# Optimization experiments

Hardware: AMD Instinct MI355X
Metric: run time of the kernel (lower is better)

The kernel has to match this reference:

```python
import jax, jax.numpy as jnp
import numpy as np

B, H, S, D = 2, 16, 2048, 128
SPARSITY = 0.1
NEG = -1.0e9


def local_mask(seq_len: int) -> jnp.ndarray:
    # window_size = max(1, int(seq_len * sparsity)); row i keeps cols [i-w//2, i+w//2]
    w = max(1, int(seq_len * SPARSITY))
    half = w // 2
    idx = jnp.arange(seq_len)
    diff = idx[None, :] - idx[:, None]  # j - i
    return ((diff >= -half) & (diff <= half)).astype(jnp.float32)


def setup_inputs() -> dict:
    key = jax.random.key(0)
    kq, kk, kv = jax.random.split(key, 3)
    return {
        "query": jax.random.normal(kq, (B, H, S, D), dtype=jnp.float32),
        "key": jax.random.normal(kk, (B, H, S, D), dtype=jnp.float32),
        "value": jax.random.normal(kv, (B, H, S, D), dtype=jnp.float32),
    }


def reference(query, key, value):
    head_dim = query.shape[-1]
    seq_len_k = key.shape[2]
    m = local_mask(seq_len_k)[None, None]  # [1,1,S,S]
    scores = jnp.einsum("bhqd,bhkd->bhqk", query, key) / jnp.sqrt(
        jnp.asarray(head_dim, query.dtype)
    )
    scores = scores * m + (1.0 - m) * NEG
    probs = jax.nn.softmax(scores, axis=-1)
    context = jnp.einsum("bhqk,bhkd->bhqd", probs, value)
    return context, probs
```

## Files before the change

kernel.cpp:

```cpp
#include <hip/hip_runtime.h>
#include <math.h>


namespace {
constexpr int Sc = 2048, Dc = 128;
constexpr int HALFW = 102;
constexpr float SCALE = 0.08838834764831845f;
constexpr int TQ  = 32;
constexpr int CT  = 256;
constexpr int KST = 136;
constexpr int VST = 132;
constexpr int PTS = 36;
constexpr int OFF_KBUF = 0;
constexpr int OFF_PST  = 34816;
constexpr int OFF_QS   = 34816;
constexpr int OFF_RED  = 34816 + 36864;
constexpr int LDS_TOTAL = OFF_RED + 512 + 128 + 128;
}

typedef __bf16 bf16x8 __attribute__((ext_vector_type(8)));
typedef float  f32x16 __attribute__((ext_vector_type(16)));
typedef float  fx4    __attribute__((ext_vector_type(4)));

__device__ __forceinline__ unsigned short f2bf(float f) {
    unsigned u = __float_as_uint(f);
    u += 0x7fffu + ((u >> 16) & 1u);
    return (unsigned short)(u >> 16);
}

__global__ __launch_bounds__(256, 2) void sparse_attn_mfma(
    const float* __restrict__ Q, const float* __restrict__ K,
    const float* __restrict__ V, float* __restrict__ ctx,
    float* __restrict__ probs)
{
    __shared__ __align__(16) unsigned char smem[LDS_TOTAL];
    unsigned short* Ks   = (unsigned short*)(smem + OFF_KBUF);
    float*          Vsf  = (float*)(smem + OFF_KBUF);
    float*          Ps_t = (float*)(smem + OFF_PST);
    unsigned short* Qs   = (unsigned short*)(smem + OFF_QS);
    float (*red)[4]      = (float(*)[4])(smem + OFF_RED);
    float* rowM          = (float*)(smem + OFF_RED + 512);
    float* rowSinv       = (float*)(smem + OFF_RED + 512 + 128);

    const int tid  = threadIdx.x;
    const int lane = tid & 63;
    const int w    = tid >> 6;
    const int lo   = lane & 31;
    const int hi   = lane >> 5;

    const int wid = (blockIdx.x & 7) * 256 + (blockIdx.x >> 3);
    const int bh  = wid >> 6;
    const int qt  = wid & 63;
    const int i0  = qt * TQ;
    const int js0 = max(0, i0 - HALFW);
    const int jend = min(js0 + CT, Sc);

    const size_t rowbase = (size_t)bh * Sc;
    float* probsBase = probs + (rowbase + i0) * (size_t)Sc;

    {
        const int headN = js0 & 3;
        const int tailN = (4 - (jend & 3)) & 3;
        const int hn = headN + tailN;
        if (hn == 4) {
            int r = tid >> 2, s = tid & 3;
            if (r < TQ) {
                int col = (s < headN) ? (js0 - headN + s) : (jend + s - headN);
                __builtin_nontemporal_store(0.0f, probsBase + (size_t)r * Sc + col);
            }
        } else if (hn == 2) {
            int r = tid >> 1, s = tid & 1;
            if (r < TQ) {
                int col = (s < headN) ? (js0 - headN + s) : (jend + s - headN);
                __builtin_nontemporal_store(0.0f, probsBase + (size_t)r * Sc + col);
            }
        }
        const int leftQ   = (js0 - headN) >> 2;
        const int rightQ0 = (jend + tailN) >> 2;
        const fx4 z4 = {0.f, 0.f, 0.f, 0.f};
        for (int r = 0; r < TQ; ++r) {
            fx4* p4 = (fx4*)(probsBase + (size_t)r * Sc);
            for (int c = tid; c < leftQ; c += 256)
                __builtin_nontemporal_store(z4, p4 + c);
            for (int c = rightQ0 + tid; c < Sc / 4; c += 256)
                __builtin_nontemporal_store(z4, p4 + c);
        }
    }

    {
        const float4* Q4 = (const float4*)(Q + (rowbase + i0) * Dc);
        #pragma unroll
        for (int it = 0; it < 4; ++it) {
            int idx = tid + 256 * it;
            int r = idx >> 5, d4 = idx & 31;
            float4 q4 = Q4[r * 32 + d4];
            ushort4 b;
            b.x = f2bf(q4.x); b.y = f2bf(q4.y); b.z = f2bf(q4.z); b.w = f2bf(q4.w);
            *(ushort4*)&Qs[r * KST + d4 * 4] = b;
        }
    }

    const float4* K4 = (const float4*)(K + rowbase * Dc);
    const float4* V4 = (const float4*)(V + rowbase * Dc);

    f32x16 accE[2];
    #pragma unroll
    for (int ch = 0; ch < 2; ++ch) {
        #pragma unroll
        for (int it = 0; it < 16; ++it) {
            int idx = tid + 256 * it;
            int r = idx >> 5, d4 = idx & 31;
            int jn = js0 + ch * 128 + r;
            if (jn > Sc - 1) jn = Sc - 1;
            float4 k4 = K4[(size_t)jn * 32 + d4];
            ushort4 b;
            b.x = f2bf(k4.x); b.y = f2bf(k4.y); b.z = f2bf(k4.z); b.w = f2bf(k4.w);
            *(ushort4*)&Ks[r * KST + d4 * 4] = b;
        }
        __syncthreads();
        f32x16 acc;
        #pragma unroll
        for (int i = 0; i < 16; ++i) acc[i] = 0.0f;
        const unsigned short* qrow = &Qs[lo * KST + hi * 8];
        const unsigned short* krow = &Ks[(w * 32 + lo) * KST + hi * 8];
        #pragma unroll
        for (int dk = 0; dk < 8; ++dk) {
            bf16x8 a = *(const bf16x8*)(qrow + dk * 16);
            bf16x8 b = *(const bf16x8*)(krow + dk * 16);
            acc = __builtin_amdgcn_mfma_f32_32x32x16_bf16(a, b, acc, 0, 0, 0);
        }
        accE[ch] = acc;
        __syncthreads();
    }

    const int cg0 = js0 + w * 32 + lo;
    {
        float mred[16];
        #pragma unroll
        for (int i = 0; i < 16; ++i) {
            int rl = (i & 3) + 8 * (i >> 2) + 4 * hi;
            int rg = i0 + rl;
            float m = -3.0e38f;
            #pragma unroll
            for (int ch = 0; ch < 2; ++ch) {
                int cg = cg0 + ch * 128;
                bool valid = (cg < Sc) & (cg >= rg - HALFW) & (cg <= rg + HALFW);
                float sv = valid ? accE[ch][i] * SCALE : -3.0e38f;
                accE[ch][i] = sv;
                m = fmaxf(m, sv);
            }
            mred[i] = m;
        }
        #pragma unroll
        for (int mk = 1; mk < 32; mk <<= 1) {
            #pragma unroll
            for (int i = 0; i < 16; ++i)
                mred[i] = fmaxf(mred[i], __shfl_xor(mred[i], mk, 64));
        }
        if (lo == 0) {
            #pragma unroll
            for (int i = 0; i < 16; ++i) {
                int rl = (i & 3) + 8 * (i >> 2) + 4 * hi;
                red[rl][w] = mred[i];
            }
        }
    }
    __syncthreads();
    if (tid < 128) {
        int rr = tid >> 2, sl = tid & 3;
        float v = red[rr][sl];
        v = fmaxf(v, __shfl_xor(v, 1, 64));
        v = fmaxf(v, __shfl_xor(v, 2, 64));
        if (sl == 0) rowM[rr] = v;
    }
    __syncthreads();

    {
        float sred[16];
        #pragma unroll
        for (int i = 0; i < 16; ++i) {
            int rl = (i & 3) + 8 * (i >> 2) + 4 * hi;
            float rm = rowM[rl];
            float e0 = __expf(accE[0][i] - rm);
            float e1 = __expf(accE[1][i] - rm);
            accE[0][i] = e0; accE[1][i] = e1;
            sred[i] = e0 + e1;
        }
        #pragma unroll
        for (int mk = 1; mk < 32; mk <<= 1) {
            #pragma unroll
            for (int i = 0; i < 16; ++i)
                sred[i] += __shfl_xor(sred[i], mk, 64);
        }
        if (lo == 0) {
            #pragma unroll
            for (int i = 0; i < 16; ++i) {
                int rl = (i & 3) + 8 * (i >> 2) + 4 * hi;
                red[rl][w] = sred[i];
            }
        }
    }
    __syncthreads();
    if (tid < 128) {
        int rr = tid >> 2, sl = tid & 3;
        float v = red[rr][sl];
        v += __shfl_xor(v, 1, 64);
        v += __shfl_xor(v, 2, 64);
        if (sl == 0) rowSinv[rr] = 1.0f / v;
    }
    __syncthreads();

    #pragma unroll
    for (int i = 0; i < 16; ++i) {
        int rl = (i & 3) + 8 * (i >> 2) + 4 * hi;
        float inv = rowSinv[rl];
        float* prow = probsBase + (size_t)rl * Sc;
        #pragma unroll
        for (int ch = 0; ch < 2; ++ch) {
            int cg = cg0 + ch * 128;
            float p = accE[ch][i] * inv;
            Ps_t[(cg - js0) * PTS + rl] = p;
            if (cg < Sc) __builtin_nontemporal_store(p, prow + cg);
        }
    }
    __syncthreads();

    const int kp  = lane & 3;
    const int dgq = (lane >> 2) & 1;
    const int rg  = lane >> 3;
    fx4 o[4][4];
    #pragma unroll
    for (int c = 0; c < 4; ++c)
        #pragma unroll
        for (int j = 0; j < 4; ++j) o[c][j] = (fx4){0.f, 0.f, 0.f, 0.f};

    #pragma unroll
    for (int ch4 = 0; ch4 < 4; ++ch4) {
        #pragma unroll
        for (int it = 0; it < 8; ++it) {
            int idx = tid + 256 * it;
            int r = idx >> 5, d4 = idx & 31;
            int jn = js0 + ch4 * 64 + r;
            if (jn > Sc - 1) jn = Sc - 1;
            float4 v4g = V4[(size_t)jn * 32 + d4];
            *(float4*)&Vsf[r * VST + d4 * 4] = v4g;
        }
        __syncthreads();
        const float* Pbase = &Ps_t[(ch4 * 64) * PTS + 4 * rg];
        const float* Vbase = &Vsf[w * 32 + dgq * 16];
        #pragma unroll 4
        for (int kk = 0; kk < 16; ++kk) {
            int k = 4 * kk + kp;
            fx4 p4 = *(const fx4*)(Pbase + k * PTS);
            const float* vr = Vbase + k * VST;
            fx4 v0 = *(const fx4*)(vr);
            fx4 v1 = *(const fx4*)(vr + 4);
            fx4 v2 = *(const fx4*)(vr + 8);
            fx4 v3 = *(const fx4*)(vr + 12);
            #pragma unroll
            for (int c = 0; c < 4; ++c) {
                float pc = p4[c];
                o[c][0] += v0 * pc;
                o[c][1] += v1 * pc;
                o[c][2] += v2 * pc;
                o[c][3] += v3 * pc;
            }
        }
        __syncthreads();
    }

    #pragma unroll
    for (int c = 0; c < 4; ++c) {
        #pragma unroll
        for (int j = 0; j < 4; ++j) {
            fx4 t = o[c][j];
            #pragma unroll
            for (int comp = 0; comp < 4; ++comp) {
                float s = t[comp];
                s += __shfl_xor(s, 1, 64);
                s += __shfl_xor(s, 2, 64);
                t[comp] = s;
            }
            o[c][j] = t;
        }
    }
    if (kp == 0) {
        #pragma unroll
        for (int c = 0; c < 4; ++c) {
            float* crow = ctx + (rowbase + i0 + 4 * rg + c) * (size_t)Dc
                        + w * 32 + dgq * 16;
            #pragma unroll
            for (int j = 0; j < 4; ++j)
                __builtin_nontemporal_store(o[c][j], (fx4*)crow + j);
        }
    }
}

extern "C" void kernel_launch(void* const* d_in, const int* in_sizes, int n_in,
                              void* d_out, int out_size, void* d_ws, size_t ws_size,
                              hipStream_t stream) {
    const float* Q = (const float*)d_in[0];
    const float* K = (const float*)d_in[1];
    const float* V = (const float*)d_in[2];
    float* out   = (float*)d_out;
    float* ctx   = out;
    float* probs = out + (size_t)2 * 16 * 2048 * 128;

    dim3 grid(2 * 16 * (Sc / TQ));
    dim3 block(256);
    sparse_attn_mfma<<<grid, block, 0, stream>>>(Q, K, V, ctx, probs);
}
```

Measured before the change: 692.9 us.

## Shrink LDS footprint and raise occupancy; keep Q in registers, store P as bf16

Q is now converted straight into MFMA A-operand registers, so its LDS staging buffer goes away. P is stored transposed in LDS as bf16, and V is streamed in 32-row chunks into a separate region, which shrinks LDS to about 35KB and allows launch bounds of 4 blocks per CU. The large zero-fill of the probs array moves to the end of the kernel so it can overlap with other blocks' compute, and barriers become a waitcnt+s_barrier asm. The trade-offs are lower precision for P in the PV product, tighter register pressure from the extra occupancy target, and more barriers from the doubled V chunk count.

```diff
diff --git a/kernel.cpp b/kernel.cpp
--- a/kernel.cpp
+++ b/kernel.cpp
@@ -11,33 +11,40 @@
 constexpr int KST = 136;
 constexpr int VST = 132;
 constexpr int PTS = 36;
-constexpr int OFF_KBUF = 0;
-constexpr int OFF_PST  = 34816;
-constexpr int OFF_QS   = 34816;
-constexpr int OFF_RED  = 34816 + 36864;
-constexpr int LDS_TOTAL = OFF_RED + 512 + 128 + 128;
+constexpr int OFF_PST = 0;
+constexpr int OFF_VSF = 18432;
+constexpr int SLAB    = 35328;
+constexpr int OFF_RED = SLAB;
+constexpr int LDS_TOTAL = SLAB + 512 + 128 + 128;
 }
 
 typedef __bf16 bf16x8 __attribute__((ext_vector_type(8)));
 typedef float  f32x16 __attribute__((ext_vector_type(16)));
 typedef float  fx4    __attribute__((ext_vector_type(4)));
+typedef unsigned short u16x8 __attribute__((ext_vector_type(8)));
+typedef unsigned short u16x4 __attribute__((ext_vector_type(4)));
 
 __device__ __forceinline__ unsigned short f2bf(float f) {
     unsigned u = __float_as_uint(f);
     u += 0x7fffu + ((u >> 16) & 1u);
     return (unsigned short)(u >> 16);
 }
-
-__global__ __launch_bounds__(256, 2) void sparse_attn_mfma(
+__device__ __forceinline__ float bf2f(unsigned short h) {
+    return __uint_as_float(((unsigned)h) << 16);
+}
+__device__ __forceinline__ void bar_lds() {
+    asm volatile("s_waitcnt lgkmcnt(0)\n\ts_barrier" ::: "memory");
+}
+
+__global__ __launch_bounds__(256, 4) void sparse_attn_mfma(
     const float* __restrict__ Q, const float* __restrict__ K,
     const float* __restrict__ V, float* __restrict__ ctx,
     float* __restrict__ probs)
 {
     __shared__ __align__(16) unsigned char smem[LDS_TOTAL];
-    unsigned short* Ks   = (unsigned short*)(smem + OFF_KBUF);
-    float*          Vsf  = (float*)(smem + OFF_KBUF);
-    float*          Ps_t = (float*)(smem + OFF_PST);
-    unsigned short* Qs   = (unsigned short*)(smem + OFF_QS);
+    unsigned short* Ks   = (unsigned short*)(smem);
+    unsigned short* Ps_t = (unsigned short*)(smem + OFF_PST);
+    float*          Vsf  = (float*)(smem + OFF_VSF);
     float (*red)[4]      = (float(*)[4])(smem + OFF_RED);
     float* rowM          = (float*)(smem + OFF_RED + 512);
     float* rowSinv       = (float*)(smem + OFF_RED + 512 + 128);
@@ -57,6 +64,213 @@
 
     const size_t rowbase = (size_t)bh * Sc;
     float* probsBase = probs + (rowbase + i0) * (size_t)Sc;
+
+    const float4* K4 = (const float4*)(K + rowbase * Dc);
+    const float4* V4 = (const float4*)(V + rowbase * Dc);
+
+    bf16x8 aq[8];
+    {
+        const float4* Q4 = (const float4*)(Q + (rowbase + i0) * Dc);
+        #pragma unroll 2
+        for (int dk = 0; dk < 8; ++dk) {
+            float4 a = Q4[lo * 32 + dk * 4 + hi * 2];
+            float4 b = Q4[lo * 32 + dk * 4 + hi * 2 + 1];
+            u16x8 t;
+            t[0] = f2bf(a.x); t[1] = f2bf(a.y); t[2] = f2bf(a.z); t[3] = f2bf(a.w);
+            t[4] = f2bf(b.x); t[5] = f2bf(b.y); t[6] = f2bf(b.z); t[7] = f2bf(b.w);
+            aq[dk] = __builtin_bit_cast(bf16x8, t);
+        }
+    }
+
+    f32x16 accE[2];
+    #pragma unroll
+    for (int ch = 0; ch < 2; ++ch) {
+        #pragma unroll 4
+        for (int it = 0; it < 16; ++it) {
+            int idx = tid + 256 * it;
+            int r = idx >> 5, d4 = idx & 31;
+            int jn = js0 + ch * 128 + r;
+            if (jn > Sc - 1) jn = Sc - 1;
+            float4 k4 = K4[(size_t)jn * 32 + d4];
+            ushort4 b;
+            b.x = f2bf(k4.x); b.y = f2bf(k4.y); b.z = f2bf(k4.z); b.w = f2bf(k4.w);
+            *(ushort4*)&Ks[r * KST + d4 * 4] = b;
+        }
+        bar_lds();
+        f32x16 acc;
+        #pragma unroll
+        for (int i = 0; i < 16; ++i) acc[i] = 0.0f;
+        const unsigned short* krow = &Ks[(w * 32 + lo) * KST + hi * 8];
+        #pragma unroll
+        for (int dk = 0; dk < 8; ++dk) {
+            bf16x8 b = *(const bf16x8*)(krow + dk * 16);
+            acc = __builtin_amdgcn_mfma_f32_32x32x16_bf16(aq[dk], b, acc, 0, 0, 0);
+        }
+        accE[ch] = acc;
+        bar_lds();
+    }
+
+    const int cg0 = js0 + w * 32 + lo;
+    {
+        float mred[16];
+        #pragma unroll
+        for (int i = 0; i < 16; ++i) {
+            int rl = (i & 3) + 8 * (i >> 2) + 4 * hi;
+            int rg = i0 + rl;
+            float m = -3.0e38f;
+            #pragma unroll
+            for (int ch = 0; ch < 2; ++ch) {
+                int cg = cg0 + ch * 128;
+                bool valid = (cg < Sc) & (cg >= rg - HALFW) & (cg <= rg + HALFW);
+                float sv = valid ? accE[ch][i] * SCALE : -3.0e38f;
+                accE[ch][i] = sv;
+                m = fmaxf(m, sv);
+            }
+            mred[i] = m;
+        }
+        #pragma unroll
+        for (int mk = 1; mk < 32; mk <<= 1) {
+            #pragma unroll
+            for (int i = 0; i < 16; ++i)
+                mred[i] = fmaxf(mred[i], __shfl_xor(mred[i], mk, 64));
+        }
+        if (lo == 0) {
+            #pragma unroll
+            for (int i = 0; i < 16; ++i) {
+                int rl = (i & 3) + 8 * (i >> 2) + 4 * hi;
+                red[rl][w] = mred[i];
+            }
+        }
+    }
+    bar_lds();
+    if (tid < 128) {
+        int rr = tid >> 2, sl = tid & 3;
+        float v = red[rr][sl];
+        v = fmaxf(v, __shfl_xor(v, 1, 64));
+        v = fmaxf(v, __shfl_xor(v, 2, 64));
+        if (sl == 0) rowM[rr] = v;
+    }
+    bar_lds();
+
+    {
+        float sred[16];
+        #pragma unroll
+        for (int i = 0; i < 16; ++i) {
+            int rl = (i & 3) + 8 * (i >> 2) + 4 * hi;
+            float rm = rowM[rl];
+            float e0 = __expf(accE[0][i] - rm);
+            float e1 = __expf(accE[1][i] - rm);
+            accE[0][i] = e0; accE[1][i] = e1;
+            sred[i] = e0 + e1;
+        }
+        #pragma unroll
+        for (int mk = 1; mk < 32; mk <<= 1) {
+            #pragma unroll
+            for (int i = 0; i < 16; ++i)
+                sred[i] += __shfl_xor(sred[i], mk, 64);
+        }
+        if (lo == 0) {
+            #pragma unroll
+            for (int i = 0; i < 16; ++i) {
+                int rl = (i & 3) + 8 * (i >> 2) + 4 * hi;
+                red[rl][w] = sred[i];
+            }
+        }
+    }
+    bar_lds();
+    if (tid < 128) {
+        int rr = tid >> 2, sl = tid & 3;
+        float v = red[rr][sl];
+        v += __shfl_xor(v, 1, 64);
+        v += __shfl_xor(v, 2, 64);
+        if (sl == 0) rowSinv[rr] = 1.0f / v;
+    }
+    bar_lds();
+
+    #pragma unroll
+    for (int i = 0; i < 16; ++i) {
+        int rl = (i & 3) + 8 * (i >> 2) + 4 * hi;
+        float inv = rowSinv[rl];
+        float* prow = probsBase + (size_t)rl * Sc;
+        #pragma unroll
+        for (int ch = 0; ch < 2; ++ch) {
+            int cg = cg0 + ch * 128;
+            float p = accE[ch][i] * inv;
+            Ps_t[(cg - js0) * PTS + rl] = f2bf(p);
+            if (cg < Sc) __builtin_nontemporal_store(p, prow + cg);
+        }
+    }
+    bar_lds();
+
+    const int kp  = lane & 3;
+    const int dgq = (lane >> 2) & 1;
+    const int rg  = lane >> 3;
+    fx4 o[4][4];
+    #pragma unroll
+    for (int c = 0; c < 4; ++c)
+        #pragma unroll
+        for (int j = 0; j < 4; ++j) o[c][j] = (fx4){0.f, 0.f, 0.f, 0.f};
+
+    #pragma unroll 2
+    for (int ch8 = 0; ch8 < 8; ++ch8) {
+        #pragma unroll
+        for (int it = 0; it < 4; ++it) {
+            int idx = tid + 256 * it;
+            int r = idx >> 5, d4 = idx & 31;
+            int jn = js0 + ch8 * 32 + r;
+            if (jn > Sc - 1) jn = Sc - 1;
+            float4 v4g = V4[(size_t)jn * 32 + d4];
+            *(float4*)&Vsf[r * VST + d4 * 4] = v4g;
+        }
+        bar_lds();
+        const unsigned short* Pbase = &Ps_t[(ch8 * 32) * PTS + 4 * rg];
+        const float* Vbase = &Vsf[w * 32 + dgq * 16];
+        #pragma unroll 4
+        for (int kk = 0; kk < 8; ++kk) {
+            int k = 4 * kk + kp;
+            u16x4 pb = *(const u16x4*)(Pbase + k * PTS);
+            const float* vr = Vbase + k * VST;
+            fx4 v0 = *(const fx4*)(vr);
+            fx4 v1 = *(const fx4*)(vr + 4);
+            fx4 v2 = *(const fx4*)(vr + 8);
+            fx4 v3 = *(const fx4*)(vr + 12);
+            #pragma unroll
+            for (int c = 0; c < 4; ++c) {
+                float pc = bf2f(pb[c]);
+                o[c][0] += v0 * pc;
+                o[c][1] += v1 * pc;
+                o[c][2] += v2 * pc;
+                o[c][3] += v3 * pc;
+            }
+        }
+        bar_lds();
+    }
+
+    #pragma unroll
+    for (int c = 0; c < 4; ++c) {
+        #pragma unroll
+        for (int j = 0; j < 4; ++j) {
+            fx4 t = o[c][j];
+            #pragma unroll
+            for (int comp = 0; comp < 4; ++comp) {
+                float s = t[comp];
+                s += __shfl_xor(s, 1, 64);
+                s += __shfl_xor(s, 2, 64);
+                t[comp] = s;
+            }
+            o[c][j] = t;
+        }
+    }
+    if (kp == 0) {
+        #pragma unroll
+        for (int c = 0; c < 4; ++c) {
+            float* crow = ctx + (rowbase + i0 + 4 * rg + c) * (size_t)Dc
+                        + w * 32 + dgq * 16;
+            #pragma unroll
+            for (int j = 0; j < 4; ++j)
+                __builtin_nontemporal_store(o[c][j], (fx4*)crow + j);
+        }
+    }
 
     {
         const int headN = js0 & 3;
@@ -86,214 +300,6 @@
                 __builtin_nontemporal_store(z4, p4 + c);
         }
     }
-
-    {
-        const float4* Q4 = (const float4*)(Q + (rowbase + i0) * Dc);
-        #pragma unroll
-        for (int it = 0; it < 4; ++it) {
-            int idx = tid + 256 * it;
-            int r = idx >> 5, d4 = idx & 31;
-            float4 q4 = Q4[r * 32 + d4];
-            ushort4 b;
-            b.x = f2bf(q4.x); b.y = f2bf(q4.y); b.z = f2bf(q4.z); b.w = f2bf(q4.w);
-            *(ushort4*)&Qs[r * KST + d4 * 4] = b;
-        }
-    }
-
-    const float4* K4 = (const float4*)(K + rowbase * Dc);
-    const float4* V4 = (const float4*)(V + rowbase * Dc);
-
-    f32x16 accE[2];
-    #pragma unroll
-    for (int ch = 0; ch < 2; ++ch) {
-        #pragma unroll
-        for (int it = 0; it < 16; ++it) {
-            int idx = tid + 256 * it;
-            int r = idx >> 5, d4 = idx & 31;
-            int jn = js0 + ch * 128 + r;
-            if (jn > Sc - 1) jn = Sc - 1;
-            float4 k4 = K4[(size_t)jn * 32 + d4];
-            ushort4 b;
-            b.x = f2bf(k4.x); b.y = f2bf(k4.y); b.z = f2bf(k4.z); b.w = f2bf(k4.w);
-            *(ushort4*)&Ks[r * KST + d4 * 4] = b;
-        }
-        __syncthreads();
-        f32x16 acc;
-        #pragma unroll
-        for (int i = 0; i < 16; ++i) acc[i] = 0.0f;
-        const unsigned short* qrow = &Qs[lo * KST + hi * 8];
-        const unsigned short* krow = &Ks[(w * 32 + lo) * KST + hi * 8];
-        #pragma unroll
-        for (int dk = 0; dk < 8; ++dk) {
-            bf16x8 a = *(const bf16x8*)(qrow + dk * 16);
-            bf16x8 b = *(const bf16x8*)(krow + dk * 16);
-            acc = __builtin_amdgcn_mfma_f32_32x32x16_bf16(a, b, acc, 0, 0, 0);
-        }
-        accE[ch] = acc;
-        __syncthreads();
-    }
-
-    const int cg0 = js0 + w * 32 + lo;
-    {
-        float mred[16];
-        #pragma unroll
-        for (int i = 0; i < 16; ++i) {
-            int rl = (i & 3) + 8 * (i >> 2) + 4 * hi;
-            int rg = i0 + rl;
-            float m = -3.0e38f;
-            #pragma unroll
-            for (int ch = 0; ch < 2; ++ch) {
-                int cg = cg0 + ch * 128;
-                bool valid = (cg < Sc) & (cg >= rg - HALFW) & (cg <= rg + HALFW);
-                float sv = valid ? accE[ch][i] * SCALE : -3.0e38f;
-                accE[ch][i] = sv;
-                m = fmaxf(m, sv);
-            }
-            mred[i] = m;
-        }
-        #pragma unroll
-        for (int mk = 1; mk < 32; mk <<= 1) {
-            #pragma unroll
-            for (int i = 0; i < 16; ++i)
-                mred[i] = fmaxf(mred[i], __shfl_xor(mred[i], mk, 64));
-        }
-        if (lo == 0) {
-            #pragma unroll
-            for (int i = 0; i < 16; ++i) {
-                int rl = (i & 3) + 8 * (i >> 2) + 4 * hi;
-                red[rl][w] = mred[i];
-            }
-        }
-    }
-    __syncthreads();
-    if (tid < 128) {
-        int rr = tid >> 2, sl = tid & 3;
-        float v = red[rr][sl];
-        v = fmaxf(v, __shfl_xor(v, 1, 64));
-        v = fmaxf(v, __shfl_xor(v, 2, 64));
-        if (sl == 0) rowM[rr] = v;
-    }
-    __syncthreads();
-
-    {
-        float sred[16];
-        #pragma unroll
-        for (int i = 0; i < 16; ++i) {
-            int rl = (i & 3) + 8 * (i >> 2) + 4 * hi;
-            float rm = rowM[rl];
-            float e0 = __expf(accE[0][i] - rm);
-            float e1 = __expf(accE[1][i] - rm);
-            accE[0][i] = e0; accE[1][i] = e1;
-            sred[i] = e0 + e1;
-        }
-        #pragma unroll
-        for (int mk = 1; mk < 32; mk <<= 1) {
-            #pragma unroll
-            for (int i = 0; i < 16; ++i)
-                sred[i] += __shfl_xor(sred[i], mk, 64);
-        }
-        if (lo == 0) {
-            #pragma unroll
-            for (int i = 0; i < 16; ++i) {
-                int rl = (i & 3) + 8 * (i >> 2) + 4 * hi;
-                red[rl][w] = sred[i];
-            }
-        }
-    }
-    __syncthreads();
-    if (tid < 128) {
-        int rr = tid >> 2, sl = tid & 3;
-        float v = red[rr][sl];
-        v += __shfl_xor(v, 1, 64);
-        v += __shfl_xor(v, 2, 64);
-        if (sl == 0) rowSinv[rr] = 1.0f / v;
-    }
-    __syncthreads();
-
-    #pragma unroll
-    for (int i = 0; i < 16; ++i) {
-        int rl = (i & 3) + 8 * (i >> 2) + 4 * hi;
-        float inv = rowSinv[rl];
-        float* prow = probsBase + (size_t)rl * Sc;
-        #pragma unroll
-        for (int ch = 0; ch < 2; ++ch) {
-            int cg = cg0 + ch * 128;
-            float p = accE[ch][i] * inv;
-            Ps_t[(cg - js0) * PTS + rl] = p;
-            if (cg < Sc) __builtin_nontemporal_store(p, prow + cg);
-        }
-    }
-    __syncthreads();
-
-    const int kp  = lane & 3;
-    const int dgq = (lane >> 2) & 1;
-    const int rg  = lane >> 3;
-    fx4 o[4][4];
-    #pragma unroll
-    for (int c = 0; c < 4; ++c)
-        #pragma unroll
-        for (int j = 0; j < 4; ++j) o[c][j] = (fx4){0.f, 0.f, 0.f, 0.f};
-
-    #pragma unroll
-    for (int ch4 = 0; ch4 < 4; ++ch4) {
-        #pragma unroll
-        for (int it = 0; it < 8; ++it) {
-            int idx = tid + 256 * it;
-            int r = idx >> 5, d4 = idx & 31;
-            int jn = js0 + ch4 * 64 + r;
-            if (jn > Sc - 1) jn = Sc - 1;
-            float4 v4g = V4[(size_t)jn * 32 + d4];
-            *(float4*)&Vsf[r * VST + d4 * 4] = v4g;
-        }
-        __syncthreads();
-        const float* Pbase = &Ps_t[(ch4 * 64) * PTS + 4 * rg];
-        const float* Vbase = &Vsf[w * 32 + dgq * 16];
-        #pragma unroll 4
-        for (int kk = 0; kk < 16; ++kk) {
-            int k = 4 * kk + kp;
-            fx4 p4 = *(const fx4*)(Pbase + k * PTS);
-            const float* vr = Vbase + k * VST;
-            fx4 v0 = *(const fx4*)(vr);
-            fx4 v1 = *(const fx4*)(vr + 4);
-            fx4 v2 = *(const fx4*)(vr + 8);
-            fx4 v3 = *(const fx4*)(vr + 12);
-            #pragma unroll
-            for (int c = 0; c < 4; ++c) {
-                float pc = p4[c];
-                o[c][0] += v0 * pc;
-                o[c][1] += v1 * pc;
-                o[c][2] += v2 * pc;
-                o[c][3] += v3 * pc;
-            }
-        }
-        __syncthreads();
-    }
-
-    #pragma unroll
-    for (int c = 0; c < 4; ++c) {
-        #pragma unroll
-        for (int j = 0; j < 4; ++j) {
-            fx4 t = o[c][j];
-            #pragma unroll
-            for (int comp = 0; comp < 4; ++comp) {
-                float s = t[comp];
-                s += __shfl_xor(s, 1, 64);
-                s += __shfl_xor(s, 2, 64);
-                t[comp] = s;
-            }
-            o[c][j] = t;
-        }
-    }
-    if (kp == 0) {
-        #pragma unroll
-        for (int c = 0; c < 4; ++c) {
-            float* crow = ctx + (rowbase + i0 + 4 * rg + c) * (size_t)Dc
-                        + w * 32 + dgq * 16;
-            #pragma unroll
-            for (int j = 0; j < 4; ++j)
-                __builtin_nontemporal_store(o[c][j], (fx4*)crow + j);
-        }
-    }
 }
 
 extern "C" void kernel_launch(void* const* d_in, const int* in_sizes, int n_in,
```

After: 797.0 us. 1.15x slower.
